# Performance work log

Measured on AMD Instinct MI355X. Metric: run time of the kernel, lower is better.

## Reference

```python
import jax, jax.numpy as jnp
import numpy as np

B, S, H, QKV, NH, MLP = 4, 2048, 512, 512, 8, 2048
HD = QKV // NH
EPS = 1e-6


def _layernorm(x):
    # LayerNorm over last dim, no affine, eps=1e-6
    mu = jnp.mean(x, axis=-1, keepdims=True)
    var = jnp.mean(jnp.square(x - mu), axis=-1, keepdims=True)
    return (x - mu) * jax.lax.rsqrt(var + EPS)


def setup_inputs() -> dict:
    key = jax.random.key(0)
    ks = jax.random.split(key, 8)
    sc_in = 1.0 / np.sqrt(H)
    sc_qkv = 1.0 / np.sqrt(QKV)
    sc_mlp = 1.0 / np.sqrt(MLP)
    return {
        "input": jax.random.normal(ks[0], (B, S, H), dtype=jnp.float32),
        "mask": jnp.ones((B, S), dtype=jnp.float32),
        "Wq": jax.random.normal(ks[1], (H, QKV), dtype=jnp.float32) * sc_in,
        "Wk": jax.random.normal(ks[2], (H, QKV), dtype=jnp.float32) * sc_in,
        "Wv": jax.random.normal(ks[3], (H, QKV), dtype=jnp.float32) * sc_in,
        "Wo": jax.random.normal(ks[4], (QKV, H), dtype=jnp.float32) * sc_qkv,
        "W1": jax.random.normal(ks[5], (H, MLP), dtype=jnp.float32) * sc_in,
        "W2": jax.random.normal(ks[6], (MLP, H), dtype=jnp.float32) * sc_mlp,
    }


def reference(input, mask, Wq, Wk, Wv, Wo, W1, W2):
    # pre-mask + pre-norm
    x = input * mask[..., None]
    x = _layernorm(x)
    # qkv projections, split heads: [B,S,QKV] -> [B,NH,S,HD]
    def heads(t):
        return t.reshape(B, S, NH, HD).transpose(0, 2, 1, 3)
    q = heads(x @ Wq) * (1.0 / np.sqrt(HD))
    k = heads(x @ Wk)
    v = heads(x @ Wv)
    logits = jnp.einsum("bhqd,bhkd->bhqk", q, k)  # [B,NH,S,S]
    amask = mask[:, None, :, None]  # 'b q -> b 1 q 1'
    logits = logits + (-100000.0) * (1.0 - amask)
    att = jax.nn.softmax(logits, axis=-1)
    out = jnp.einsum("bhqk,bhkd->bhqd", att, v)
    out = out.transpose(0, 2, 1, 3).reshape(B, S, QKV)
    x = input + out @ Wo  # residual
    x = x * mask[..., None]
    y = _layernorm(x)
    ffn = jax.nn.gelu(y @ W1, approximate=False) @ W2
    return ffn + x
```

## Files before the change

kernel.cpp:

```cpp
#include <hip/hip_runtime.h>
#include <hip/hip_bf16.h>
#include <cmath>

typedef __attribute__((ext_vector_type(8))) short bf16x8;
typedef __attribute__((ext_vector_type(4))) float f32x4;
typedef __attribute__((ext_vector_type(16))) float f32x16;
typedef unsigned short u16;
typedef unsigned int u32;

#define B_ 4
#define S_ 2048
#define H_ 512
#define NH_ 8
#define HD_ 64
#define MLP_ 2048
#define M_ (B_*S_)

__device__ __forceinline__ float bf2f(u16 u){ u32 v=((u32)u)<<16; float f; __builtin_memcpy(&f,&v,4); return f; }
__device__ __forceinline__ u16 f2bf(float f){ u32 u; __builtin_memcpy(&u,&f,4); u32 r=(u+0x7fffu+((u>>16)&1u))>>16; return (u16)r; }
__device__ __forceinline__ u32 pk2(float lo, float hi2){
  __hip_bfloat162 t = __float22bfloat162_rn(make_float2(lo, hi2));
  u32 r; __builtin_memcpy(&r, &t, 4); return r;
}

__device__ __forceinline__ float xhalf_add(float x){
  float a = x, b = x;
  asm volatile("v_permlane32_swap_b32 %0, %1" : "+v"(a), "+v"(b));
  return a + b;
}
__device__ __forceinline__ float xhalf_max(float x){
  float a = x, b = x;
  asm volatile("v_permlane32_swap_b32 %0, %1" : "+v"(a), "+v"(b));
  return fmaxf(a, b);
}

__device__ __forceinline__ void gl16(const u16* g, u16* l) {
  __builtin_amdgcn_global_load_lds((const __attribute__((address_space(1))) u32*)(g),
                                   (__attribute__((address_space(3))) u32*)(l), 16, 0, 0);
}

__device__ __forceinline__ void gemm_core(
    const u16* __restrict__ A, const u16* __restrict__ Bt,
    int lda, int ldb, int nkt, int m0, int n0,
    u16* As, u16* Bs, f32x4 (&acc)[4][4])
{
  const int tid = threadIdx.x;
  const int lane = tid & 63;
  const int w = tid >> 6;
  const int lr = lane & 15;
  const int g  = lane >> 4;
  const int wr = w >> 1, wc = w & 1;

  int srow[2], scol[2], soff[2];
#pragma unroll
  for (int c = 0; c < 2; ++c) {
    int off = (w*2+c)*512 + lane*8;
    int row = off >> 5;
    int gl  = (off >> 3) & 3;
    srow[c] = row;
    scol[c] = ((gl ^ ((row>>1)&3)) << 3);
    soff[c] = (w*2+c)*512;
  }
  int aoff[4], boff[4];
#pragma unroll
  for (int m = 0; m < 4; ++m) {
    int ra = wr*64 + m*16 + lr;
    aoff[m] = ra*32 + ((g ^ ((ra>>1)&3))<<3);
    int rb = wc*64 + m*16 + lr;
    boff[m] = rb*32 + ((g ^ ((rb>>1)&3))<<3);
  }
  const u16* Ap = A + (size_t)m0*lda;
  const u16* Bp = Bt + (size_t)n0*ldb;

#pragma unroll
  for (int c = 0; c < 2; ++c) {
    gl16(Ap + (size_t)srow[c]*lda + scol[c], As + soff[c]);
    gl16(Bp + (size_t)srow[c]*ldb + scol[c], Bs + soff[c]);
  }

  for (int kt = 0; kt < nkt; ++kt) {
    const int cb = (kt & 1) * 4096;
    if (kt + 1 < nkt) {
      const int k0 = (kt + 1) << 5;
      const int nb = ((kt + 1) & 1) * 4096;
#pragma unroll
      for (int c = 0; c < 2; ++c) {
        gl16(Ap + (size_t)srow[c]*lda + k0 + scol[c], As + nb + soff[c]);
        gl16(Bp + (size_t)srow[c]*ldb + k0 + scol[c], Bs + nb + soff[c]);
      }
      asm volatile("s_waitcnt vmcnt(4)" ::: "memory");
    } else {
      asm volatile("s_waitcnt vmcnt(0)" ::: "memory");
    }
    __builtin_amdgcn_s_barrier();

    bf16x8 af[4], bfr[4];
#pragma unroll
    for (int m = 0; m < 4; ++m) {
      af[m]  = *(const bf16x8*)(As + cb + aoff[m]);
      bfr[m] = *(const bf16x8*)(Bs + cb + boff[m]);
    }
#pragma unroll
    for (int m = 0; m < 4; ++m) {
#pragma unroll
      for (int n = 0; n < 4; ++n) {
        acc[m][n] = __builtin_amdgcn_mfma_f32_16x16x32_bf16(af[m], bfr[n], acc[m][n], 0, 0, 0);
      }
    }
    __builtin_amdgcn_s_barrier();
  }
}

__device__ __forceinline__ void gemm_core64(
    const u16* __restrict__ A, const u16* __restrict__ Bt,
    int lda, int ldb, int nkt, int m0, int n0,
    u16* As, u16* Bs, f32x4 (&acc)[2][4])
{
  const int tid = threadIdx.x;
  const int lane = tid & 63;
  const int w = tid >> 6;
  const int lr = lane & 15;
  const int g  = lane >> 4;

  int srow[2], scol[2], soff[2];
#pragma unroll
  for (int c = 0; c < 2; ++c) {
    int off = (w*2+c)*512 + lane*8;
    int row = off >> 5;
    int gl  = (off >> 3) & 3;
    srow[c] = row;
    scol[c] = ((gl ^ ((row>>1)&3)) << 3);
    soff[c] = (w*2+c)*512;
  }
  int offB = w*512 + lane*8;
  int srowB = offB >> 5;
  int scolB = ((((offB>>3)&3) ^ ((srowB>>1)&3)) << 3);
  int soffB = w*512;

  int aoff[2], boff[4];
#pragma unroll
  for (int m = 0; m < 2; ++m) {
    int ra = w*32 + m*16 + lr;
    aoff[m] = ra*32 + ((g ^ ((ra>>1)&3))<<3);
  }
#pragma unroll
  for (int n = 0; n < 4; ++n) {
    int rb = n*16 + lr;
    boff[n] = rb*32 + ((g ^ ((rb>>1)&3))<<3);
  }
  const u16* Ap = A + (size_t)m0*lda;
  const u16* Bp = Bt + (size_t)n0*ldb;

#pragma unroll
  for (int c = 0; c < 2; ++c) gl16(Ap + (size_t)srow[c]*lda + scol[c], As + soff[c]);
  gl16(Bp + (size_t)srowB*ldb + scolB, Bs + soffB);

  for (int kt = 0; kt < nkt; ++kt) {
    const int cbA = (kt & 1) * 4096;
    const int cbB = (kt & 1) * 2048;
    if (kt + 1 < nkt) {
      const int k0 = (kt + 1) << 5;
      const int nbA = ((kt + 1) & 1) * 4096;
      const int nbB = ((kt + 1) & 1) * 2048;
#pragma unroll
      for (int c = 0; c < 2; ++c) gl16(Ap + (size_t)srow[c]*lda + k0 + scol[c], As + nbA + soff[c]);
      gl16(Bp + (size_t)srowB*ldb + k0 + scolB, Bs + nbB + soffB);
      asm volatile("s_waitcnt vmcnt(3)" ::: "memory");
    } else {
      asm volatile("s_waitcnt vmcnt(0)" ::: "memory");
    }
    __builtin_amdgcn_s_barrier();

    bf16x8 af[2], bfr[4];
#pragma unroll
    for (int m = 0; m < 2; ++m) af[m] = *(const bf16x8*)(As + cbA + aoff[m]);
#pragma unroll
    for (int n = 0; n < 4; ++n) bfr[n] = *(const bf16x8*)(Bs + cbB + boff[n]);
#pragma unroll
    for (int m = 0; m < 2; ++m) {
#pragma unroll
      for (int n = 0; n < 4; ++n) {
        acc[m][n] = __builtin_amdgcn_mfma_f32_16x16x32_bf16(af[m], bfr[n], acc[m][n], 0, 0, 0);
      }
    }
    __builtin_amdgcn_s_barrier();
  }
}

__global__ __launch_bounds__(256,2) void k_qkv(
    const u16* __restrict__ xn, const u16* __restrict__ wqt,
    const u16* __restrict__ wkt, const u16* __restrict__ wvt,
    u16* __restrict__ q, u16* __restrict__ k, u16* __restrict__ v)
{
  __shared__ u16 As[2*128*32], Bs[2*128*32];
  int m0 = blockIdx.x*128;
  int sel = blockIdx.y >> 2;
  int n0 = (blockIdx.y & 3)*128;
  const u16* Bt = sel==0 ? wqt : (sel==1 ? wkt : wvt);
  u16* O = sel==0 ? q : (sel==1 ? k : v);
  float alpha = (sel==0) ? 0.125f : 1.0f;
  f32x4 acc[4][4] = {};
  gemm_core(xn, Bt, H_, H_, H_/32, m0, n0, As, Bs, acc);
  const int lane = threadIdx.x&63, w = threadIdx.x>>6;
  const int lr = lane&15, g = lane>>4, wr = w>>1, wc = w&1;
#pragma unroll
  for (int m=0;m<4;++m) {
#pragma unroll
    for (int n=0;n<4;++n) {
#pragma unroll
      for (int r=0;r<4;++r) {
        int row = m0 + wr*64 + m*16 + g*4 + r;
        int col = n0 + wc*64 + n*16 + lr;
        O[(size_t)row*H_ + col] = f2bf(acc[m][n][r]*alpha);
      }
    }
  }
}

template<int EPI>
__global__ __launch_bounds__(256,2) void k_gemm(
    const u16* __restrict__ A, const u16* __restrict__ Bt, void* __restrict__ Ov,
    const float* __restrict__ aux, const float* __restrict__ maskv,
    int N, int K)
{
  __shared__ u16 As[2*128*32], Bs[2*128*32];
  int m0 = blockIdx.x*128, n0 = blockIdx.y*128;
  f32x4 acc[4][4] = {};
  gemm_core(A, Bt, K, K, K>>5, m0, n0, As, Bs, acc);
  const int lane = threadIdx.x&63, w = threadIdx.x>>6;
  const int lr = lane&15, g = lane>>4, wr = w>>1, wc = w&1;
#pragma unroll
  for (int m=0;m<4;++m) {
#pragma unroll
    for (int n=0;n<4;++n) {
#pragma unroll
      for (int r=0;r<4;++r) {
        int row = m0 + wr*64 + m*16 + g*4 + r;
        int col = n0 + wc*64 + n*16 + lr;
        float val = acc[m][n][r];
        if (EPI == 1) {
          val = 0.5f*val*(1.0f + erff(val*0.70710678118654752f));
          ((u16*)Ov)[(size_t)row*N + col] = f2bf(val);
        } else if (EPI == 2) {
          float mv = maskv[row];
          val = (aux[(size_t)row*N + col] + val)*mv;
          ((float*)Ov)[(size_t)row*N + col] = val;
        } else if (EPI == 3) {
          val += aux[(size_t)row*N + col];
          ((float*)Ov)[(size_t)row*N + col] = val;
        }
      }
    }
  }
}

template<int EPI>
__global__ __launch_bounds__(256,2) void k_gemm64(
    const u16* __restrict__ A, const u16* __restrict__ Bt, void* __restrict__ Ov,
    const float* __restrict__ aux, const float* __restrict__ maskv,
    int N, int K)
{
  __shared__ u16 As[2*128*32], Bs[2*64*32];
  int m0 = blockIdx.x*128, n0 = blockIdx.y*64;
  f32x4 acc[2][4] = {};
  gemm_core64(A, Bt, K, K, K>>5, m0, n0, As, Bs, acc);
  const int lane = threadIdx.x&63, w = threadIdx.x>>6;
  const int lr = lane&15, g = lane>>4;
#pragma unroll
  for (int m=0;m<2;++m) {
#pragma unroll
    for (int n=0;n<4;++n) {
#pragma unroll
      for (int r=0;r<4;++r) {
        int row = m0 + w*32 + m*16 + g*4 + r;
        int col = n0 + n*16 + lr;
        float val = acc[m][n][r];
        if (EPI == 2) {
          float mv = maskv[row];
          val = (aux[(size_t)row*N + col] + val)*mv;
          ((float*)Ov)[(size_t)row*N + col] = val;
        } else if (EPI == 3) {
          val += aux[(size_t)row*N + col];
          ((float*)Ov)[(size_t)row*N + col] = val;
        }
      }
    }
  }
}

template<int MASKED>
__global__ __launch_bounds__(256) void k_ln(const float* __restrict__ in,
    const float* __restrict__ mask, u16* __restrict__ out)
{
  int row = blockIdx.x*4 + (threadIdx.x>>6);
  int lane = threadIdx.x & 63;
  const f32x4* p = (const f32x4*)(in + (size_t)row*H_ + lane*8);
  f32x4 a = p[0], b = p[1];
  float mv = MASKED ? mask[row] : 1.0f;
  float x[8]; float s = 0.f, s2 = 0.f;
#pragma unroll
  for (int j=0;j<4;++j){ x[j] = a[j]*mv; x[4+j] = b[j]*mv; }
#pragma unroll
  for (int j=0;j<8;++j){ s += x[j]; s2 += x[j]*x[j]; }
#pragma unroll
  for (int m=1;m<32;m<<=1){ s += __shfl_xor(s,m); s2 += __shfl_xor(s2,m); }
  s = xhalf_add(s); s2 = xhalf_add(s2);
  float mu = s*(1.0f/H_);
  float var = s2*(1.0f/H_) - mu*mu;
  float inv = rsqrtf(var + 1e-6f);
  bf16x8 o;
#pragma unroll
  for (int j=0;j<8;++j) o[j] = (short)f2bf((x[j]-mu)*inv);
  *(bf16x8*)(out + (size_t)row*H_ + lane*8) = o;
}

__global__ void k_tr4(const float* __restrict__ s0, const float* __restrict__ s1,
                      const float* __restrict__ s2, const float* __restrict__ s3,
                      u16* __restrict__ d0, u16* __restrict__ d1,
                      u16* __restrict__ d2, u16* __restrict__ d3)
{
  __shared__ u16 t[32][33];
  const float* src = blockIdx.z==0 ? s0 : (blockIdx.z==1 ? s1 : (blockIdx.z==2 ? s2 : s3));
  u16* dst = blockIdx.z==0 ? d0 : (blockIdx.z==1 ? d1 : (blockIdx.z==2 ? d2 : d3));
  int c0 = blockIdx.x*32, r0 = blockIdx.y*32;
  int tx = threadIdx.x & 31, ty = threadIdx.x >> 5;
#pragma unroll
  for (int i=0;i<32;i+=8) t[ty+i][tx] = f2bf(src[(size_t)(r0+ty+i)*512 + c0+tx]);
  __syncthreads();
#pragma unroll
  for (int i=0;i<32;i+=8) dst[(size_t)(c0+ty+i)*512 + r0+tx] = t[tx][ty+i];
}

__global__ void k_tr(const float* __restrict__ src, u16* __restrict__ dst, int R, int C)
{
  __shared__ u16 t[32][33];
  int c0 = blockIdx.x*32, r0 = blockIdx.y*32;
  int tx = threadIdx.x & 31, ty = threadIdx.x >> 5;
#pragma unroll
  for (int i=0;i<32;i+=8) t[ty+i][tx] = f2bf(src[(size_t)(r0+ty+i)*C + c0+tx]);
  __syncthreads();
#pragma unroll
  for (int i=0;i<32;i+=8) dst[(size_t)(c0+ty+i)*R + r0+tx] = t[tx][ty+i];
}

__global__ void k_trv(const u16* __restrict__ v, u16* __restrict__ vt)
{
  __shared__ u16 t[32][33];
  int bh = blockIdx.z, b = bh>>3, h = bh&7;
  int s0 = blockIdx.x*32, d0 = blockIdx.y*32;
  int tx = threadIdx.x & 31, ty = threadIdx.x >> 5;
#pragma unroll
  for (int i=0;i<32;i+=8) t[ty+i][tx] = v[(size_t)(b*S_ + s0+ty+i)*H_ + h*HD_ + d0+tx];
  __syncthreads();
#pragma unroll
  for (int i=0;i<32;i+=8) vt[((size_t)bh*HD_ + d0+ty+i)*S_ + s0+tx] = t[tx][ty+i];
}

__global__ __launch_bounds__(256) void k_attn(
    const u16* __restrict__ q, const u16* __restrict__ kmat,
    const u16* __restrict__ vt, const float* __restrict__ mask,
    u16* __restrict__ o)
{
  __shared__ u16 Ks[2][64*64];
  __shared__ u16 Vs[2][64*64];
  __shared__ float bias[S_];
  __shared__ float lsums[4][32];

  const int tid = threadIdx.x;
  const int lane = tid & 63;
  const int w = tid >> 6;
  const int l31 = lane & 31;
  const int hi = lane >> 5;
  const int bh = blockIdx.y, b = bh >> 3, h = bh & 7;
  const int q0 = blockIdx.x * 128;

  const int sr = lane >> 3;
  const int sl = (lane & 7) ^ (sr & 7);
  const u16* ks0 = kmat + (size_t)(b*S_ + w*16 + sr)*H_ + h*HD_ + sl*8;
  const u16* ks1 = ks0 + (size_t)8*H_;
  const u16* vs0 = vt + ((size_t)bh*HD_ + w*16 + sr)*S_ + sl*8;
  const u16* vs1 = vs0 + (size_t)8*S_;

  {
    u16* kd = &Ks[0][0] + w*1024;
    u16* vd = &Vs[0][0] + w*1024;
    gl16(ks0, kd); gl16(ks1, kd + 512);
    gl16(vs0, vd); gl16(vs1, vd + 512);
  }

  for (int j = tid; j < S_; j += 256) bias[j] = -100000.0f * (1.0f - mask[b*S_ + j]);

  bf16x8 qf[4];
  {
    const u16* qp = q + (size_t)(b*S_ + q0 + w*32 + l31)*H_ + h*HD_ + hi*8;
#pragma unroll
    for (int ds = 0; ds < 4; ++ds) qf[ds] = *(const bf16x8*)(qp + ds*16);
  }

  f32x16 po0 = {}, po1 = {};
  float mreg = -1e30f, lsum = 0.f;

  __syncthreads();

  for (int jt = 0; jt < 32; ++jt) {
    const int buf = jt & 1;
    if (jt < 31) {
      const int j0 = (jt + 1) * 64;
      u16* kd = &Ks[buf ^ 1][0] + w*1024;
      u16* vd = &Vs[buf ^ 1][0] + w*1024;
      gl16(ks0 + (size_t)j0*H_, kd); gl16(ks1 + (size_t)j0*H_, kd + 512);
      gl16(vs0 + j0, vd);            gl16(vs1 + j0, vd + 512);
      asm volatile("s_waitcnt vmcnt(4)" ::: "memory");
    } else {
      asm volatile("s_waitcnt vmcnt(0)" ::: "memory");
    }
    __builtin_amdgcn_s_barrier();

    const u16* kt  = &Ks[buf][0];
    const u16* vtl = &Vs[buf][0];

    f32x16 s0, s1;
    const float* bp = &bias[jt*64 + hi*4];
#pragma unroll
    for (int kb = 0; kb < 2; ++kb) {
      f32x16 acc;
#pragma unroll
      for (int g2 = 0; g2 < 4; ++g2) {
        f32x4 b4 = *(const f32x4*)(bp + kb*32 + g2*8);
        acc[g2*4+0] = b4[0]; acc[g2*4+1] = b4[1];
        acc[g2*4+2] = b4[2]; acc[g2*4+3] = b4[3];
      }
      const int key = kb*32 + l31;
      const u16* kr = kt + key*64;
      __builtin_amdgcn_s_setprio(1);
#pragma unroll
      for (int ds = 0; ds < 4; ++ds) {
        bf16x8 kf = *(const bf16x8*)(kr + (((ds*2 + hi) ^ (key & 7)) << 3));
        acc = __builtin_amdgcn_mfma_f32_32x32x16_bf16(kf, qf[ds], acc, 0, 0, 0);
      }
      __builtin_amdgcn_s_setprio(0);
      if (kb == 0) s0 = acc; else s1 = acc;
    }

    float g0 = fmaxf(fmaxf(fmaxf(s0[0], s0[1]), fmaxf(s0[2], s0[3])),
                     fmaxf(fmaxf(s1[0], s1[1]), fmaxf(s1[2], s1[3])));
    float g1 = fmaxf(fmaxf(fmaxf(s0[4], s0[5]), fmaxf(s0[6], s0[7])),
                     fmaxf(fmaxf(s1[4], s1[5]), fmaxf(s1[6], s1[7])));
    float g2 = fmaxf(fmaxf(fmaxf(s0[8], s0[9]), fmaxf(s0[10], s0[11])),
                     fmaxf(fmaxf(s1[8], s1[9]), fmaxf(s1[10], s1[11])));
    float g3 = fmaxf(fmaxf(fmaxf(s0[12], s0[13]), fmaxf(s0[14], s0[15])),
                     fmaxf(fmaxf(s1[12], s1[13]), fmaxf(s1[14], s1[15])));
    float mx = xhalf_max(fmaxf(fmaxf(g0, g1), fmaxf(g2, g3)));
    if (__any(mx > mreg + 8.0f)) {
      float mn = fmaxf(mreg, mx);
      float sc = __expf(mreg - mn);
      lsum *= sc;
#pragma unroll
      for (int r = 0; r < 16; ++r) { po0[r] *= sc; po1[r] *= sc; }
      mreg = mn;
    }
#pragma unroll
    for (int r = 0; r < 16; ++r) {
      s0[r] = __expf(s0[r]-mreg);
      s1[r] = __expf(s1[r]-mreg);
    }
    float h0 = ((s0[0]+s0[1])+(s0[2]+s0[3])) + ((s1[0]+s1[1])+(s1[2]+s1[3]));
    float h1 = ((s0[4]+s0[5])+(s0[6]+s0[7])) + ((s1[4]+s1[5])+(s1[6]+s1[7]));
    float h2 = ((s0[8]+s0[9])+(s0[10]+s0[11])) + ((s1[8]+s1[9])+(s1[10]+s1[11]));
    float h3 = ((s0[12]+s0[13])+(s0[14]+s0[15])) + ((s1[12]+s1[13])+(s1[14]+s1[15]));
    lsum += xhalf_add((h0+h1)+(h2+h3));

#pragma unroll
    for (int kb = 0; kb < 2; ++kb) {
      const f32x16& sv = kb ? s1 : s0;
      u32 w01 = pk2(sv[0],  sv[1]);
      u32 w23 = pk2(sv[2],  sv[3]);
      u32 w45 = pk2(sv[4],  sv[5]);
      u32 w67 = pk2(sv[6],  sv[7]);
      asm volatile("v_permlane32_swap_b32 %0, %1" : "+v"(w01), "+v"(w45));
      asm volatile("v_permlane32_swap_b32 %0, %1" : "+v"(w23), "+v"(w67));
      u32 w89 = pk2(sv[8],  sv[9]);
      u32 wab = pk2(sv[10], sv[11]);
      u32 wcd = pk2(sv[12], sv[13]);
      u32 wef = pk2(sv[14], sv[15]);
      asm volatile("v_permlane32_swap_b32 %0, %1" : "+v"(w89), "+v"(wcd));
      asm volatile("v_permlane32_swap_b32 %0, %1" : "+v"(wab), "+v"(wef));
      union { u32 wrd[4]; bf16x8 v; } f0, f1;
      f0.wrd[0]=w01; f0.wrd[1]=w23; f0.wrd[2]=w45; f0.wrd[3]=w67;
      f1.wrd[0]=w89; f1.wrd[1]=wab; f1.wrd[2]=wcd; f1.wrd[3]=wef;
      __builtin_amdgcn_s_setprio(1);
#pragma unroll
      for (int ks = 0; ks < 2; ++ks) {
        bf16x8 pa = ks ? f1.v : f0.v;
#pragma unroll
        for (int nb = 0; nb < 2; ++nb) {
          int dd = nb*32 + l31;
          int slot = ((kb*4 + ks*2 + hi) ^ (dd & 7)) << 3;
          bf16x8 vf = *(const bf16x8*)(vtl + dd*64 + slot);
          if (nb == 0) po0 = __builtin_amdgcn_mfma_f32_32x32x16_bf16(pa, vf, po0, 0,0,0);
          else         po1 = __builtin_amdgcn_mfma_f32_32x32x16_bf16(pa, vf, po1, 0,0,0);
        }
      }
      __builtin_amdgcn_s_setprio(0);
    }
    __builtin_amdgcn_s_barrier();
  }

  if (hi == 0) lsums[w][l31] = lsum;
  f32x4 li[4];
#pragma unroll
  for (int g2i = 0; g2i < 4; ++g2i) {
    f32x4 t = *(const f32x4*)&lsums[w][g2i*8 + hi*4];
    li[g2i][0] = 1.0f/t[0]; li[g2i][1] = 1.0f/t[1];
    li[g2i][2] = 1.0f/t[2]; li[g2i][3] = 1.0f/t[3];
  }
  u16* op = o + (size_t)(b*S_ + q0 + w*32)*H_ + h*HD_;
#pragma unroll
  for (int nb = 0; nb < 2; ++nb) {
#pragma unroll
    for (int r = 0; r < 16; ++r) {
      int row = (r&3) + 8*(r>>2) + 4*hi;
      float val = (nb ? po1[r] : po0[r]) * li[r>>2][r&3];
      op[(size_t)row*H_ + nb*32 + l31] = f2bf(val);
    }
  }
}

extern "C" void kernel_launch(void* const* d_in, const int* in_sizes, int n_in,
                              void* d_out, int out_size, void* d_ws, size_t ws_size,
                              hipStream_t stream) {
  const float* input = (const float*)d_in[0];
  const float* mask  = (const float*)d_in[1];
  const float* Wq = (const float*)d_in[2];
  const float* Wk = (const float*)d_in[3];
  const float* Wv = (const float*)d_in[4];
  const float* Wo = (const float*)d_in[5];
  const float* W1 = (const float*)d_in[6];
  const float* W2 = (const float*)d_in[7];
  float* out = (float*)d_out;
  u16* ws = (u16*)d_ws;

  u16* wqt = ws;
  u16* wkt = wqt + 262144;
  u16* wvt = wkt + 262144;
  u16* wot = wvt + 262144;
  u16* w1t = wot + 262144;
  u16* w2t = w1t + 1048576;
  u16* xn  = w2t + 1048576;
  u16* q   = xn  + 4194304;
  u16* k   = q   + 4194304;
  u16* v   = k   + 4194304;
  u16* vt  = v   + 4194304;
  u16*   attn = xn;
  float* x2f  = (float*)q;
  u16*   y    = v;
  u16*   h1   = vt;

  dim3 blk(256);
  k_tr4<<<dim3(16,16,4), blk, 0, stream>>>(Wq, Wk, Wv, Wo, wqt, wkt, wvt, wot);
  k_tr<<<dim3(64,16), blk, 0, stream>>>(W1, w1t, 512, 2048);
  k_tr<<<dim3(16,64), blk, 0, stream>>>(W2, w2t, 2048, 512);

  k_ln<1><<<2048, blk, 0, stream>>>(input, mask, xn);
  k_qkv<<<dim3(64,12), blk, 0, stream>>>(xn, wqt, wkt, wvt, q, k, v);
  k_trv<<<dim3(64,2,32), blk, 0, stream>>>(v, vt);
  k_attn<<<dim3(16,32), blk, 0, stream>>>(q, k, vt, mask, attn);
  k_gemm64<2><<<dim3(64,8), blk, 0, stream>>>(attn, wot, (void*)x2f, input, mask, 512, 512);
  k_ln<0><<<2048, blk, 0, stream>>>(x2f, nullptr, y);
  k_gemm<1><<<dim3(64,16), blk, 0, stream>>>(y, w1t, (void*)h1, nullptr, nullptr, 2048, 512);
  k_gemm64<3><<<dim3(64,8), blk, 0, stream>>>(h1, w2t, (void*)out, x2f, nullptr, 512, 2048);
}
```

Baseline: 194.9 us.

## Double GEMM K-tile to 64, raise gemm64 occupancy, simplify softmax reductions

The GEMM cores now stage 64-wide K tiles instead of 32 in LDS, using a new 8-way XOR swizzle and two MFMA sub-steps per tile. This halves the number of barrier and wait rounds per GEMM at the cost of twice the LDS. The k_gemm64 launch bound is raised to 3 blocks per CU. In attention, the tree max/sum reductions and permlane32 swaps are replaced by serial loops and __shfl_xor, which yields longer dependency chains and possibly slower LDS-based shuffles.

```diff
diff --git a/kernel.cpp b/kernel.cpp
--- a/kernel.cpp
+++ b/kernel.cpp
@@ -28,11 +28,6 @@
   asm volatile("v_permlane32_swap_b32 %0, %1" : "+v"(a), "+v"(b));
   return a + b;
 }
-__device__ __forceinline__ float xhalf_max(float x){
-  float a = x, b = x;
-  asm volatile("v_permlane32_swap_b32 %0, %1" : "+v"(a), "+v"(b));
-  return fmaxf(a, b);
-}
 
 __device__ __forceinline__ void gl16(const u16* g, u16* l) {
   __builtin_amdgcn_global_load_lds((const __attribute__((address_space(1))) u32*)(g),
@@ -51,60 +46,59 @@
   const int g  = lane >> 4;
   const int wr = w >> 1, wc = w & 1;
 
-  int srow[2], scol[2], soff[2];
-#pragma unroll
-  for (int c = 0; c < 2; ++c) {
-    int off = (w*2+c)*512 + lane*8;
-    int row = off >> 5;
-    int gl  = (off >> 3) & 3;
-    srow[c] = row;
-    scol[c] = ((gl ^ ((row>>1)&3)) << 3);
-    soff[c] = (w*2+c)*512;
-  }
-  int aoff[4], boff[4];
+  const int sr = lane >> 3;
+  const int scol = ((lane & 7) ^ sr) << 3;
+
+  int aoff[2][4], boff[2][4];
 #pragma unroll
   for (int m = 0; m < 4; ++m) {
     int ra = wr*64 + m*16 + lr;
-    aoff[m] = ra*32 + ((g ^ ((ra>>1)&3))<<3);
     int rb = wc*64 + m*16 + lr;
-    boff[m] = rb*32 + ((g ^ ((rb>>1)&3))<<3);
+#pragma unroll
+    for (int kk = 0; kk < 2; ++kk) {
+      aoff[kk][m] = ra*64 + (((kk*4+g) ^ (ra&7))<<3);
+      boff[kk][m] = rb*64 + (((kk*4+g) ^ (rb&7))<<3);
+    }
   }
   const u16* Ap = A + (size_t)m0*lda;
   const u16* Bp = Bt + (size_t)n0*ldb;
 
 #pragma unroll
-  for (int c = 0; c < 2; ++c) {
-    gl16(Ap + (size_t)srow[c]*lda + scol[c], As + soff[c]);
-    gl16(Bp + (size_t)srow[c]*ldb + scol[c], Bs + soff[c]);
+  for (int c = 0; c < 4; ++c) {
+    gl16(Ap + (size_t)(w*32 + c*8 + sr)*lda + scol, As + w*2048 + c*512);
+    gl16(Bp + (size_t)(w*32 + c*8 + sr)*ldb + scol, Bs + w*2048 + c*512);
   }
 
   for (int kt = 0; kt < nkt; ++kt) {
-    const int cb = (kt & 1) * 4096;
+    const int cb = (kt & 1) * 8192;
     if (kt + 1 < nkt) {
-      const int k0 = (kt + 1) << 5;
-      const int nb = ((kt + 1) & 1) * 4096;
-#pragma unroll
-      for (int c = 0; c < 2; ++c) {
-        gl16(Ap + (size_t)srow[c]*lda + k0 + scol[c], As + nb + soff[c]);
-        gl16(Bp + (size_t)srow[c]*ldb + k0 + scol[c], Bs + nb + soff[c]);
-      }
-      asm volatile("s_waitcnt vmcnt(4)" ::: "memory");
+      const int k0 = (kt + 1) << 6;
+      const int nb = ((kt + 1) & 1) * 8192;
+#pragma unroll
+      for (int c = 0; c < 4; ++c) {
+        gl16(Ap + (size_t)(w*32 + c*8 + sr)*lda + k0 + scol, As + nb + w*2048 + c*512);
+        gl16(Bp + (size_t)(w*32 + c*8 + sr)*ldb + k0 + scol, Bs + nb + w*2048 + c*512);
+      }
+      asm volatile("s_waitcnt vmcnt(8)" ::: "memory");
     } else {
       asm volatile("s_waitcnt vmcnt(0)" ::: "memory");
     }
     __builtin_amdgcn_s_barrier();
 
-    bf16x8 af[4], bfr[4];
-#pragma unroll
-    for (int m = 0; m < 4; ++m) {
-      af[m]  = *(const bf16x8*)(As + cb + aoff[m]);
-      bfr[m] = *(const bf16x8*)(Bs + cb + boff[m]);
-    }
-#pragma unroll
-    for (int m = 0; m < 4; ++m) {
-#pragma unroll
-      for (int n = 0; n < 4; ++n) {
-        acc[m][n] = __builtin_amdgcn_mfma_f32_16x16x32_bf16(af[m], bfr[n], acc[m][n], 0, 0, 0);
+#pragma unroll
+    for (int kk = 0; kk < 2; ++kk) {
+      bf16x8 af[4], bfr[4];
+#pragma unroll
+      for (int m = 0; m < 4; ++m) {
+        af[m]  = *(const bf16x8*)(As + cb + aoff[kk][m]);
+        bfr[m] = *(const bf16x8*)(Bs + cb + boff[kk][m]);
+      }
+#pragma unroll
+      for (int m = 0; m < 4; ++m) {
+#pragma unroll
+        for (int n = 0; n < 4; ++n) {
+          acc[m][n] = __builtin_amdgcn_mfma_f32_16x16x32_bf16(af[m], bfr[n], acc[m][n], 0, 0, 0);
+        }
       }
     }
     __builtin_amdgcn_s_barrier();
@@ -122,65 +116,64 @@
   const int lr = lane & 15;
   const int g  = lane >> 4;
 
-  int srow[2], scol[2], soff[2];
-#pragma unroll
-  for (int c = 0; c < 2; ++c) {
-    int off = (w*2+c)*512 + lane*8;
-    int row = off >> 5;
-    int gl  = (off >> 3) & 3;
-    srow[c] = row;
-    scol[c] = ((gl ^ ((row>>1)&3)) << 3);
-    soff[c] = (w*2+c)*512;
-  }
-  int offB = w*512 + lane*8;
-  int srowB = offB >> 5;
-  int scolB = ((((offB>>3)&3) ^ ((srowB>>1)&3)) << 3);
-  int soffB = w*512;
-
-  int aoff[2], boff[4];
+  const int sr = lane >> 3;
+  const int scol = ((lane & 7) ^ sr) << 3;
+
+  int aoff[2][2], boff[2][4];
 #pragma unroll
   for (int m = 0; m < 2; ++m) {
     int ra = w*32 + m*16 + lr;
-    aoff[m] = ra*32 + ((g ^ ((ra>>1)&3))<<3);
+#pragma unroll
+    for (int kk = 0; kk < 2; ++kk) aoff[kk][m] = ra*64 + (((kk*4+g) ^ (ra&7))<<3);
   }
 #pragma unroll
   for (int n = 0; n < 4; ++n) {
     int rb = n*16 + lr;
-    boff[n] = rb*32 + ((g ^ ((rb>>1)&3))<<3);
+#pragma unroll
+    for (int kk = 0; kk < 2; ++kk) boff[kk][n] = rb*64 + (((kk*4+g) ^ (rb&7))<<3);
   }
   const u16* Ap = A + (size_t)m0*lda;
   const u16* Bp = Bt + (size_t)n0*ldb;
 
 #pragma unroll
-  for (int c = 0; c < 2; ++c) gl16(Ap + (size_t)srow[c]*lda + scol[c], As + soff[c]);
-  gl16(Bp + (size_t)srowB*ldb + scolB, Bs + soffB);
+  for (int c = 0; c < 4; ++c)
+    gl16(Ap + (size_t)(w*32 + c*8 + sr)*lda + scol, As + w*2048 + c*512);
+#pragma unroll
+  for (int c = 0; c < 2; ++c)
+    gl16(Bp + (size_t)(w*16 + c*8 + sr)*ldb + scol, Bs + w*1024 + c*512);
 
   for (int kt = 0; kt < nkt; ++kt) {
-    const int cbA = (kt & 1) * 4096;
-    const int cbB = (kt & 1) * 2048;
+    const int cbA = (kt & 1) * 8192;
+    const int cbB = (kt & 1) * 4096;
     if (kt + 1 < nkt) {
-      const int k0 = (kt + 1) << 5;
-      const int nbA = ((kt + 1) & 1) * 4096;
-      const int nbB = ((kt + 1) & 1) * 2048;
-#pragma unroll
-      for (int c = 0; c < 2; ++c) gl16(Ap + (size_t)srow[c]*lda + k0 + scol[c], As + nbA + soff[c]);
-      gl16(Bp + (size_t)srowB*ldb + k0 + scolB, Bs + nbB + soffB);
-      asm volatile("s_waitcnt vmcnt(3)" ::: "memory");
+      const int k0 = (kt + 1) << 6;
+      const int nbA = ((kt + 1) & 1) * 8192;
+      const int nbB = ((kt + 1) & 1) * 4096;
+#pragma unroll
+      for (int c = 0; c < 4; ++c)
+        gl16(Ap + (size_t)(w*32 + c*8 + sr)*lda + k0 + scol, As + nbA + w*2048 + c*512);
+#pragma unroll
+      for (int c = 0; c < 2; ++c)
+        gl16(Bp + (size_t)(w*16 + c*8 + sr)*ldb + k0 + scol, Bs + nbB + w*1024 + c*512);
+      asm volatile("s_waitcnt vmcnt(6)" ::: "memory");
     } else {
       asm volatile("s_waitcnt vmcnt(0)" ::: "memory");
     }
     __builtin_amdgcn_s_barrier();
 
-    bf16x8 af[2], bfr[4];
-#pragma unroll
-    for (int m = 0; m < 2; ++m) af[m] = *(const bf16x8*)(As + cbA + aoff[m]);
-#pragma unroll
-    for (int n = 0; n < 4; ++n) bfr[n] = *(const bf16x8*)(Bs + cbB + boff[n]);
-#pragma unroll
-    for (int m = 0; m < 2; ++m) {
-#pragma unroll
-      for (int n = 0; n < 4; ++n) {
-        acc[m][n] = __builtin_amdgcn_mfma_f32_16x16x32_bf16(af[m], bfr[n], acc[m][n], 0, 0, 0);
+#pragma unroll
+    for (int kk = 0; kk < 2; ++kk) {
+      bf16x8 af[2], bfr[4];
+#pragma unroll
+      for (int m = 0; m < 2; ++m) af[m] = *(const bf16x8*)(As + cbA + aoff[kk][m]);
+#pragma unroll
+      for (int n = 0; n < 4; ++n) bfr[n] = *(const bf16x8*)(Bs + cbB + boff[kk][n]);
+#pragma unroll
+      for (int m = 0; m < 2; ++m) {
+#pragma unroll
+        for (int n = 0; n < 4; ++n) {
+          acc[m][n] = __builtin_amdgcn_mfma_f32_16x16x32_bf16(af[m], bfr[n], acc[m][n], 0, 0, 0);
+        }
       }
     }
     __builtin_amdgcn_s_barrier();
@@ -192,7 +185,7 @@
     const u16* __restrict__ wkt, const u16* __restrict__ wvt,
     u16* __restrict__ q, u16* __restrict__ k, u16* __restrict__ v)
 {
-  __shared__ u16 As[2*128*32], Bs[2*128*32];
+  __shared__ u16 As[2*128*64], Bs[2*128*64];
   int m0 = blockIdx.x*128;
   int sel = blockIdx.y >> 2;
   int n0 = (blockIdx.y & 3)*128;
@@ -200,7 +193,7 @@
   u16* O = sel==0 ? q : (sel==1 ? k : v);
   float alpha = (sel==0) ? 0.125f : 1.0f;
   f32x4 acc[4][4] = {};
-  gemm_core(xn, Bt, H_, H_, H_/32, m0, n0, As, Bs, acc);
+  gemm_core(xn, Bt, H_, H_, H_/64, m0, n0, As, Bs, acc);
   const int lane = threadIdx.x&63, w = threadIdx.x>>6;
   const int lr = lane&15, g = lane>>4, wr = w>>1, wc = w&1;
 #pragma unroll
@@ -223,10 +216,10 @@
     const float* __restrict__ aux, const float* __restrict__ maskv,
     int N, int K)
 {
-  __shared__ u16 As[2*128*32], Bs[2*128*32];
+  __shared__ u16 As[2*128*64], Bs[2*128*64];
   int m0 = blockIdx.x*128, n0 = blockIdx.y*128;
   f32x4 acc[4][4] = {};
-  gemm_core(A, Bt, K, K, K>>5, m0, n0, As, Bs, acc);
+  gemm_core(A, Bt, K, K, K>>6, m0, n0, As, Bs, acc);
   const int lane = threadIdx.x&63, w = threadIdx.x>>6;
   const int lr = lane&15, g = lane>>4, wr = w>>1, wc = w&1;
 #pragma unroll
@@ -255,15 +248,15 @@
 }
 
 template<int EPI>
-__global__ __launch_bounds__(256,2) void k_gemm64(
+__global__ __launch_bounds__(256,3) void k_gemm64(
     const u16* __restrict__ A, const u16* __restrict__ Bt, void* __restrict__ Ov,
     const float* __restrict__ aux, const float* __restrict__ maskv,
     int N, int K)
 {
-  __shared__ u16 As[2*128*32], Bs[2*64*32];
+  __shared__ u16 As[2*128*64], Bs[2*64*64];
   int m0 = blockIdx.x*128, n0 = blockIdx.y*64;
   f32x4 acc[2][4] = {};
-  gemm_core64(A, Bt, K, K, K>>5, m0, n0, As, Bs, acc);
+  gemm_core64(A, Bt, K, K, K>>6, m0, n0, As, Bs, acc);
   const int lane = threadIdx.x&63, w = threadIdx.x>>6;
   const int lr = lane&15, g = lane>>4;
 #pragma unroll
@@ -442,15 +435,12 @@
       if (kb == 0) s0 = acc; else s1 = acc;
     }
 
-    float g0 = fmaxf(fmaxf(fmaxf(s0[0], s0[1]), fmaxf(s0[2], s0[3])),
-                     fmaxf(fmaxf(s1[0], s1[1]), fmaxf(s1[2], s1[3])));
-    float g1 = fmaxf(fmaxf(fmaxf(s0[4], s0[5]), fmaxf(s0[6], s0[7])),
-                     fmaxf(fmaxf(s1[4], s1[5]), fmaxf(s1[6], s1[7])));
-    float g2 = fmaxf(fmaxf(fmaxf(s0[8], s0[9]), fmaxf(s0[10], s0[11])),
-                     fmaxf(fmaxf(s1[8], s1[9]), fmaxf(s1[10], s1[11])));
-    float g3 = fmaxf(fmaxf(fmaxf(s0[12], s0[13]), fmaxf(s0[14], s0[15])),
-                     fmaxf(fmaxf(s1[12], s1[13]), fmaxf(s1[14], s1[15])));
-    float mx = xhalf_max(fmaxf(fmaxf(g0, g1), fmaxf(g2, g3)));
+    float mx = s0[0];
+#pragma unroll
+    for (int r = 1; r < 16; ++r) mx = fmaxf(mx, s0[r]);
+#pragma unroll
+    for (int r = 0; r < 16; ++r) mx = fmaxf(mx, s1[r]);
+    mx = fmaxf(mx, __shfl_xor(mx, 32));
     if (__any(mx > mreg + 8.0f)) {
       float mn = fmaxf(mreg, mx);
       float sc = __expf(mreg - mn);
@@ -459,16 +449,13 @@
       for (int r = 0; r < 16; ++r) { po0[r] *= sc; po1[r] *= sc; }
       mreg = mn;
     }
-#pragma unroll
-    for (int r = 0; r < 16; ++r) {
-      s0[r] = __expf(s0[r]-mreg);
-      s1[r] = __expf(s1[r]-mreg);
-    }
-    float h0 = ((s0[0]+s0[1])+(s0[2]+s0[3])) + ((s1[0]+s1[1])+(s1[2]+s1[3]));
-    float h1 = ((s0[4]+s0[5])+(s0[6]+s0[7])) + ((s1[4]+s1[5])+(s1[6]+s1[7]));
-    float h2 = ((s0[8]+s0[9])+(s0[10]+s0[11])) + ((s1[8]+s1[9])+(s1[10]+s1[11]));
-    float h3 = ((s0[12]+s0[13])+(s0[14]+s0[15])) + ((s1[12]+s1[13])+(s1[14]+s1[15]));
-    lsum += xhalf_add((h0+h1)+(h2+h3));
+    float ps = 0.f;
+#pragma unroll
+    for (int r = 0; r < 16; ++r) { float p = __expf(s0[r]-mreg); s0[r] = p; ps += p; }
+#pragma unroll
+    for (int r = 0; r < 16; ++r) { float p = __expf(s1[r]-mreg); s1[r] = p; ps += p; }
+    ps += __shfl_xor(ps, 32);
+    lsum += ps;
 
 #pragma unroll
     for (int kb = 0; kb < 2; ++kb) {
```

Result: no change. 192.7 us (-1.2%).
